# Kernel tuning notes

Measured on AMD Instinct MI355X. Metric: run time of the kernel, lower is better.

Reference implementation:

```python
import jax, jax.numpy as jnp
import numpy as np

B, S, DIM, H, D = 4, 2048, 1024, 16, 64
WINDOW = 512  # max_mem_segments * window_size


def _rotary_angles(seq_len, dim_head):
    inv_freq = 1.0 / (10000.0 ** (jnp.arange(0, dim_head, 2, dtype=jnp.float32) / dim_head))
    freqs = jnp.arange(seq_len, dtype=jnp.float32)[:, None] * inv_freq[None, :]  # [S, D/2]
    return jnp.repeat(freqs, 2, axis=-1)  # [S, D] interleaved


def _rotate_half(x):
    x1 = x[..., 0::2]
    x2 = x[..., 1::2]
    return jnp.stack((-x2, x1), axis=-1).reshape(x.shape)


def _apply_rotary(x, angles):
    # x: [b h n d], angles: [n d]
    return x * jnp.cos(angles) + _rotate_half(x) * jnp.sin(angles)


def setup_inputs() -> dict:
    key = jax.random.key(0)
    ks = jax.random.split(key, 7)
    tokens = jax.random.normal(ks[0], (B, S, DIM), dtype=jnp.float32)
    value_residual = jax.random.normal(ks[1], (B, H, S, D), dtype=jnp.float32)
    s = 0.02
    Wq = jax.random.normal(ks[2], (DIM, H * D), dtype=jnp.float32) * s
    Wkv = jax.random.normal(ks[3], (DIM, 2 * H * D), dtype=jnp.float32) * s
    Wout = jax.random.normal(ks[4], (H * D, DIM), dtype=jnp.float32) * s
    Wgate = jax.random.normal(ks[5], (DIM, H), dtype=jnp.float32) * s
    Wmix = jax.random.normal(ks[6], (DIM, H), dtype=jnp.float32) * s
    return {"tokens": tokens, "value_residual": value_residual, "Wq": Wq,
            "Wkv": Wkv, "Wout": Wout, "Wgate": Wgate, "Wmix": Wmix}


def reference(tokens, value_residual, Wq, Wkv, Wout, Wgate, Wmix):
    b, n, dim = tokens.shape
    scale = D ** -0.5

    def split_heads(t):  # [b n (h d)] -> [b h n d]
        return t.reshape(b, n, H, D).transpose(0, 2, 1, 3)

    q = split_heads(tokens @ Wq)
    kv = tokens @ Wkv
    k = split_heads(kv[..., : H * D])
    v = split_heads(kv[..., H * D:])

    q = q * scale

    # value-residual lerp: v.lerp(value_residual, mix)
    mix = jax.nn.sigmoid(jnp.einsum('bnd,dh->bhn', tokens, Wmix))[..., None]  # [b h n 1]
    v = v + (value_residual - v) * mix

    angles = _rotary_angles(n, D)
    q = _apply_rotary(q, angles)
    k = _apply_rotary(k, angles)

    sim = jnp.einsum('bhid,bhjd->bhij', q, k)

    # fixed-window causal mask: dist = i - j; masked if dist < 0 or dist > WINDOW
    pos = jnp.arange(n)
    dist = pos[:, None] - pos[None, :]
    mask = (dist < 0) | (dist > WINDOW)
    neg = -jnp.finfo(sim.dtype).max
    sim = jnp.where(mask[None, None], neg, sim)

    attn = jax.nn.softmax(sim, axis=-1)
    out = jnp.einsum('bhij,bhjd->bhid', attn, v)

    gates = jax.nn.sigmoid(jnp.einsum('bnd,dh->bhn', tokens, Wgate))[..., None]  # [b h n 1]
    out = out * gates

    out = out.transpose(0, 2, 1, 3).reshape(b, n, H * D)
    return out @ Wout
```

## Files before the change

kernel.cpp:

```cpp
#include <hip/hip_runtime.h>

#define NH 16
#define SLEN 2048
#define DMODEL 1024
#define DHEAD 64
#define WIN 512
#define NB 4

typedef unsigned short u16;
typedef unsigned int u32;
typedef unsigned long long u64;
typedef __attribute__((ext_vector_type(8))) __bf16 bf16x8;
typedef __attribute__((ext_vector_type(4))) float floatx4;

__device__ __forceinline__ float b2f(u32 bits16) {
  union { u32 i; float f; } x; x.i = bits16 << 16; return x.f;
}
__device__ __forceinline__ u16 f2b(float f) {
  union { float f; u32 i; } x; x.f = f;
  u32 r = x.i + 0x7fffu + ((x.i >> 16) & 1u);
  return (u16)(r >> 16);
}

__device__ __forceinline__ void gl2lds16(const u16* g, u16* l) {
  __builtin_amdgcn_global_load_lds(
      (const __attribute__((address_space(1))) unsigned int*)g,
      (__attribute__((address_space(3))) unsigned int*)l, 16, 0, 0);
}

template<int OFF>
__device__ __forceinline__ bf16x8 ldsr128(u32 addr) {
  bf16x8 r;
  if constexpr (OFF == 0)
    asm volatile("ds_read_b128 %0, %1" : "=v"(r) : "v"(addr));
  else
    asm volatile("ds_read_b128 %0, %1 offset:%2" : "=v"(r) : "v"(addr), "i"(OFF));
  return r;
}

#define WAIT_VM6   asm volatile("s_waitcnt vmcnt(6)" ::: "memory")
#define WAIT_VM0   asm volatile("s_waitcnt vmcnt(0)" ::: "memory")
#define WAIT_LGKM8 asm volatile("s_waitcnt lgkmcnt(8)" ::: "memory")
#define WAIT_LGKM0 asm volatile("s_waitcnt lgkmcnt(0)" ::: "memory")

__global__ __launch_bounds__(256) void prep_all(
    const float* __restrict__ tokens, const float* __restrict__ Wq,
    const float* __restrict__ Wkv, const float* __restrict__ Wout,
    const float* __restrict__ Wmix, const float* __restrict__ Wgate,
    u64* __restrict__ tokA64, u16* __restrict__ WqkvT, u16* __restrict__ WoutT,
    u16* __restrict__ Wmg, float2* __restrict__ rtab) {
  __shared__ u16 T[64][72];
  const int blk = blockIdx.x, tid = threadIdx.x;
  if (blk < 8192) {
    int i = blk * 256 + tid;
    float4 f = reinterpret_cast<const float4*>(tokens)[i];
    union { u16 u[4]; u64 ll; } pk;
    pk.u[0] = f2b(f.x); pk.u[1] = f2b(f.y); pk.u[2] = f2b(f.z); pk.u[3] = f2b(f.w);
    tokA64[i] = pk.ll;
  } else if (blk < 9216) {
    const float* src; u16* dst; int ld, nb, n0, k0;
    if (blk < 8960) {
      int tile = blk - 8192;
      n0 = (tile % 48) * 64; k0 = (tile / 48) * 64;
      if (n0 < 1024) { src = Wq; ld = 1024; nb = n0; }
      else { src = Wkv; ld = 2048; nb = n0 - 1024; }
      dst = WqkvT;
    } else {
      int tile = blk - 8960;
      n0 = (tile % 16) * 64; k0 = (tile / 16) * 64;
      src = Wout; ld = 1024; nb = n0; dst = WoutT;
    }
#pragma unroll
    for (int i = 0; i < 16; ++i) {
      int e = i * 256 + tid;
      int kr = e >> 6, nc = e & 63;
      T[kr][nc] = f2b(src[(size_t)(k0 + kr) * ld + nb + nc]);
    }
    __syncthreads();
#pragma unroll
    for (int i = 0; i < 16; ++i) {
      int e = i * 256 + tid;
      int nr = e >> 6, kc = e & 63;
      dst[(size_t)(n0 + nr) * 1024 + k0 + kc] = T[kc][nr];
    }
  } else if (blk < 9344) {
    int idx = (blk - 9216) * 256 + tid;
    int n = idx >> 10, k = idx & 1023;
    float v = (n < 16) ? Wmix[k * 16 + n] : Wgate[k * 16 + (n - 16)];
    Wmg[idx] = f2b(v);
  } else {
    int idx = (blk - 9344) * 256 + tid;
    int s = idx >> 5, t = idx & 31;
    float inv = __expf((float)t * -0.2878231366f);
    float ang = (float)s * inv;
    float sn, cs;
    __sincosf(ang, &sn, &cs);
    rtab[idx] = make_float2(cs, sn);
  }
}

__global__ __launch_bounds__(256) void mixgate_mfma(const u16* __restrict__ A,
    const u16* __restrict__ Wmg, float* __restrict__ mixws, float* __restrict__ gatews) {
  const int lane = threadIdx.x & 63, w = threadIdx.x >> 6;
  const int lm = lane & 15, quad = lane >> 4;
  const int row0 = (blockIdx.x * 4 + w) * 32;

  floatx4 acc[2][2];
#pragma unroll
  for (int i = 0; i < 2; ++i)
#pragma unroll
    for (int j = 0; j < 2; ++j)
      acc[i][j] = (floatx4){0.f, 0.f, 0.f, 0.f};

#pragma unroll 4
  for (int k0 = 0; k0 < 1024; k0 += 32) {
    bf16x8 af[2], bf[2];
#pragma unroll
    for (int mt = 0; mt < 2; ++mt)
      af[mt] = *reinterpret_cast<const bf16x8*>(
          &A[(size_t)(row0 + mt * 16 + lm) * 1024 + k0 + quad * 8]);
#pragma unroll
    for (int nt = 0; nt < 2; ++nt)
      bf[nt] = *reinterpret_cast<const bf16x8*>(
          &Wmg[(size_t)(nt * 16 + lm) * 1024 + k0 + quad * 8]);
#pragma unroll
    for (int mt = 0; mt < 2; ++mt)
#pragma unroll
      for (int nt = 0; nt < 2; ++nt)
        acc[mt][nt] = __builtin_amdgcn_mfma_f32_16x16x32_bf16(af[mt], bf[nt], acc[mt][nt], 0, 0, 0);
  }

#pragma unroll
  for (int mt = 0; mt < 2; ++mt)
#pragma unroll
    for (int r = 0; r < 4; ++r) {
      int grow = row0 + mt * 16 + quad * 4 + r;
      int b = grow >> 11, s = grow & 2047;
#pragma unroll
      for (int nt = 0; nt < 2; ++nt) {
        int n = nt * 16 + lm;
        float sig = 1.0f / (1.0f + __expf(-acc[mt][nt][r]));
        int h = n & 15;
        (n < 16 ? mixws : gatews)[(b * NH + h) * SLEN + s] = sig;
      }
    }
}

template<int MODE>
__global__ __launch_bounds__(512, 2) void gemm_pipe(
    const u16* __restrict__ A, const u16* __restrict__ Bt,
    float* __restrict__ C,
    u16* __restrict__ qws, u16* __restrict__ kws, u16* __restrict__ vws,
    const float* __restrict__ vres, const float* __restrict__ mixws,
    const float2* __restrict__ rtab, int N) {
  __shared__ u16 smem[73728];
  const int tid = threadIdx.x;
  const int nbx = N >> 7;
  const int wg = (blockIdx.x & 7) * (gridDim.x >> 3) + (blockIdx.x >> 3);
  const int bx = wg % nbx, by = wg / nbx;
  const int row0 = by * 256, col0 = bx * 128;
  const int w = tid >> 6, lane = tid & 63;
  const int wr = (w >> 1) * 64, wc = (w & 1) * 64;
  const int lm = lane & 15, quad = lane >> 4;
  const int NT = 16;
  const int sr = tid >> 3, sc = tid & 7;
  const int sl0 = (sr * 8 + sc) * 8;
  const u16* gA = A + (size_t)(row0 + sr) * 1024 + ((sc ^ (sr & 7)) << 3);
  const u16* gB = Bt + (size_t)(col0 + sr) * 1024 + ((sc ^ (sr & 7)) << 3);

  const u32 ldsbase = (u32)(size_t)(__attribute__((address_space(3))) u16*)smem;
  u32 arow[2], brow[2];
#pragma unroll
  for (int j = 0; j < 2; ++j) {
    u32 cslot = (u32)((j * 4 + quad) ^ (lm & 7));
    arow[j] = (u32)(wr + lm) * 128 + cslot * 16;
    brow[j] = (u32)(wc + lm) * 128 + cslot * 16;
  }

  floatx4 acc[4][4];
#pragma unroll
  for (int i = 0; i < 4; ++i)
#pragma unroll
    for (int j = 0; j < 4; ++j)
      acc[i][j] = (floatx4){0.f, 0.f, 0.f, 0.f};

  auto stage3 = [&](u16* Sa, u16* Sb, int ks, int half) {
    if (half == 0) {
      gl2lds16(gA + ks, Sa + sl0);
      gl2lds16(gA + 65536 + ks, Sa + 4096 + sl0);
      gl2lds16(gB + ks, Sb + sl0);
    } else {
      gl2lds16(gA + 131072 + ks, Sa + 8192 + sl0);
      gl2lds16(gA + 196608 + ks, Sa + 12288 + sl0);
      gl2lds16(gB + 65536 + ks, Sb + 4096 + sl0);
    }
  };

#pragma unroll
  for (int tt = 0; tt < 2; ++tt) {
    u16* Sa = smem + tt * 24576;
    u16* Sb = Sa + 16384;
    stage3(Sa, Sb, tt * 64, 0);
    stage3(Sa, Sb, tt * 64, 1);
  }

  int cur = 0;
  for (int t = 0; t < NT; ++t) {
    int sidx = cur + 2; if (sidx >= 3) sidx -= 3;
    u16* Sa = smem + sidx * 24576;
    u16* Sb = Sa + 16384;
    const int ks = (t + 2) << 6;
    const bool do_stage = t < NT - 2;
    const u32 abase = ldsbase + (u32)cur * 49152u;

    if (t < NT - 1) { WAIT_VM6; } else { WAIT_VM0; }
    __builtin_amdgcn_s_barrier();

    const u32 a0 = abase + arow[0], b0 = abase + 32768u + brow[0];
    const u32 a1 = abase + arow[1], b1 = abase + 32768u + brow[1];
    bf16x8 af0[4], bf0[4], af1[4], bf1[4];
    af0[0] = ldsr128<0>(a0);    af0[1] = ldsr128<2048>(a0);
    af0[2] = ldsr128<4096>(a0); af0[3] = ldsr128<6144>(a0);
    bf0[0] = ldsr128<0>(b0);    bf0[1] = ldsr128<2048>(b0);
    bf0[2] = ldsr128<4096>(b0); bf0[3] = ldsr128<6144>(b0);
    af1[0] = ldsr128<0>(a1);    af1[1] = ldsr128<2048>(a1);
    af1[2] = ldsr128<4096>(a1); af1[3] = ldsr128<6144>(a1);
    bf1[0] = ldsr128<0>(b1);    bf1[1] = ldsr128<2048>(b1);
    bf1[2] = ldsr128<4096>(b1); bf1[3] = ldsr128<6144>(b1);
    if (do_stage) { stage3(Sa, Sb, ks, 0); stage3(Sa, Sb, ks, 1); }
    __builtin_amdgcn_sched_barrier(0);
    WAIT_LGKM8;
    __builtin_amdgcn_sched_barrier(0);
    __builtin_amdgcn_s_setprio(1);
#pragma unroll
    for (int mt = 0; mt < 4; ++mt)
#pragma unroll
      for (int nt = 0; nt < 4; ++nt)
        acc[mt][nt] = __builtin_amdgcn_mfma_f32_16x16x32_bf16(
            af0[mt], bf0[nt], acc[mt][nt], 0, 0, 0);
    __builtin_amdgcn_s_setprio(0);
    WAIT_LGKM0;
    __builtin_amdgcn_sched_barrier(0);
    __builtin_amdgcn_s_setprio(1);
#pragma unroll
    for (int mt = 0; mt < 4; ++mt)
#pragma unroll
      for (int nt = 0; nt < 4; ++nt)
        acc[mt][nt] = __builtin_amdgcn_mfma_f32_16x16x32_bf16(
            af1[mt], bf1[nt], acc[mt][nt], 0, 0, 0);
    __builtin_amdgcn_s_setprio(0);

    cur += 1; if (cur >= 3) cur -= 3;
  }

  if (MODE == 0) {
#pragma unroll
    for (int mt = 0; mt < 4; ++mt)
#pragma unroll
      for (int r = 0; r < 4; ++r) {
        int grow = row0 + wr + mt * 16 + quad * 4 + r;
#pragma unroll
        for (int nt = 0; nt < 4; ++nt)
          C[(size_t)grow * N + col0 + wc + nt * 16 + lm] = acc[mt][nt][r];
      }
  } else {
    const int seg = col0 >> 10;
    if (seg < 2) {
      u16* dst = seg ? kws : qws;
      const float qs = seg ? 1.0f : 0.125f;
      const int colb = (col0 & 1023) + wc;
#pragma unroll
      for (int mt = 0; mt < 4; ++mt)
#pragma unroll
        for (int r = 0; r < 4; ++r) {
          int sg = row0 + wr + mt * 16 + quad * 4 + r;
          int b = sg >> 11, s = sg & 2047;
#pragma unroll
          for (int nt = 0; nt < 4; ++nt) {
            int nn = colb + nt * 16 + lm;
            int h = nn >> 6, d = nn & 63;
            float val = acc[mt][nt][r] * qs;
            float2 cs = rtab[(s << 5) + (d >> 1)];
            float partner = __shfl_xor(val, 1);
            float o = (d & 1) ? fmaf(val, cs.x, partner * cs.y)
                              : fmaf(val, cs.x, -partner * cs.y);
            dst[((size_t)((b * NH + h) * SLEN + s)) * 64 + d] = f2b(o);
          }
        }
    } else {
      const int h0 = (col0 - 2048) >> 6;
      const int p = (w & 1);
      const int b = row0 >> 11, s0 = row0 & 2047;
      const int bh = b * NH + h0 + p;
      u16 (*Vt)[264] = reinterpret_cast<u16(*)[264]>(smem + p * 16896);
      __syncthreads();
#pragma unroll
      for (int mt = 0; mt < 4; ++mt)
#pragma unroll
        for (int nt = 0; nt < 4; ++nt) {
          const int d = nt * 16 + lm;
          const int sl = wr + mt * 16 + quad * 4;
          union { u16 u[4]; u64 ll; } pk;
#pragma unroll
          for (int r = 0; r < 4; ++r) {
            int s = s0 + sl + r;
            float val = acc[mt][nt][r];
            float mv = mixws[bh * SLEN + s];
            float o = val + (vres[((size_t)(bh * SLEN + s)) * 64 + d] - val) * mv;
            pk.u[r] = f2b(o);
          }
          *reinterpret_cast<u64*>(&Vt[d][sl]) = pk.ll;
        }
      __syncthreads();
#pragma unroll
      for (int it = 0; it < 8; ++it) {
        int idx = it * 512 + tid;
        int ph = idx >> 11, rem = idx & 2047;
        int d = rem >> 5, ch = rem & 31;
        const u16* src = smem + ph * 16896 + d * 264 + ch * 8;
        u16* dst = vws + ((size_t)((b * NH + h0 + ph) * 64 + d)) * SLEN + s0 + ch * 8;
        *reinterpret_cast<uint4*>(dst) = *reinterpret_cast<const uint4*>(src);
      }
    }
  }
}

__global__ __launch_bounds__(256) void attn_mfma_kernel(
    const u16* __restrict__ q, const u16* __restrict__ k, const u16* __restrict__ vt,
    const float* __restrict__ gate, u16* __restrict__ X) {
  __shared__ u16 Ks[4096];
  __shared__ u16 Vs[4096];
  __shared__ u16 Ps[4][16][72];
  const int tid = threadIdx.x;
  const int w = tid >> 6, lane = tid & 63;
  const int lm = lane & 15, quad = lane >> 4;
  const int blk = blockIdx.x;
  const int qt = blk & 31;
  const int h = (blk >> 5) & 15;
  const int b = blk >> 9;
  const int bh = b * NH + h;
  const int q0 = qt * 64;
  const size_t kqbase = (size_t)bh * SLEN * 64;
  const size_t vbase  = (size_t)bh * 64 * SLEN;

  bf16x8 qf[2];
  {
    const u16* qrow = q + kqbase + (size_t)(q0 + w * 16 + lm) * 64;
    qf[0] = *reinterpret_cast<const bf16x8*>(qrow + quad * 8);
    qf[1] = *reinterpret_cast<const bf16x8*>(qrow + 32 + quad * 8);
  }

  floatx4 o[4];
#pragma unroll
  for (int nt = 0; nt < 4; ++nt) o[nt] = (floatx4){0.f, 0.f, 0.f, 0.f};
  float lsum = 0.f;
  const int iq = q0 + w * 16 + lm;

  const int c_first = (q0 >= WIN) ? ((q0 - WIN) >> 6) : 0;
  const int c_last = q0 >> 6;
  const int vrow = tid >> 3, vcol = (tid & 7) * 8;
  for (int c = c_first; c <= c_last; ++c) {
    const int c0 = c << 6;
    __syncthreads();
    {
      const u16* kg = k + kqbase + (size_t)c0 * 64;
      gl2lds16(kg + tid * 8, Ks + tid * 8);
      gl2lds16(kg + 2048 + tid * 8, Ks + 2048 + tid * 8);
      const u16* vg = vt + vbase + c0;
      gl2lds16(vg + (size_t)vrow * SLEN + vcol, Vs + tid * 8);
      gl2lds16(vg + (size_t)(vrow + 32) * SLEN + vcol, Vs + 2048 + tid * 8);
    }
    __syncthreads();

    floatx4 st[4];
#pragma unroll
    for (int mt = 0; mt < 4; ++mt) {
      bf16x8 kf0 = *reinterpret_cast<const bf16x8*>(&Ks[(mt * 16 + lm) * 64 + quad * 8]);
      bf16x8 kf1 = *reinterpret_cast<const bf16x8*>(&Ks[(mt * 16 + lm) * 64 + 32 + quad * 8]);
      st[mt] = __builtin_amdgcn_mfma_f32_16x16x32_bf16(kf0, qf[0],
                   (floatx4){0.f, 0.f, 0.f, 0.f}, 0, 0, 0);
      st[mt] = __builtin_amdgcn_mfma_f32_16x16x32_bf16(kf1, qf[1], st[mt], 0, 0, 0);
    }
    const bool need_mask = (c == c_first && q0 >= WIN) || (c == c_last);
    if (need_mask) {
#pragma unroll
      for (int mt = 0; mt < 4; ++mt)
#pragma unroll
        for (int r = 0; r < 4; ++r) {
          int j = c0 + mt * 16 + quad * 4 + r;
          bool valid = (j <= iq) && (j >= iq - WIN);
          if (!valid) st[mt][r] = -3.0e38f;
        }
    }
    float p[4][4], psum = 0.f;
#pragma unroll
    for (int mt = 0; mt < 4; ++mt)
#pragma unroll
      for (int r = 0; r < 4; ++r) {
        p[mt][r] = __expf(st[mt][r]);
        psum += p[mt][r];
      }
    psum += __shfl_xor(psum, 16);
    psum += __shfl_xor(psum, 32);
    lsum += psum;
#pragma unroll
    for (int mt = 0; mt < 4; ++mt) {
      union { u16 u[4]; u64 ll; } pk;
#pragma unroll
      for (int r = 0; r < 4; ++r) pk.u[r] = f2b(p[mt][r]);
      *reinterpret_cast<u64*>(&Ps[w][lm][mt * 16 + quad * 4]) = pk.ll;
    }
    __builtin_amdgcn_wave_barrier();
    __builtin_amdgcn_s_waitcnt(0xC07F);
    __builtin_amdgcn_wave_barrier();
    bf16x8 af0 = *reinterpret_cast<const bf16x8*>(&Ps[w][lm][quad * 8]);
    bf16x8 af1 = *reinterpret_cast<const bf16x8*>(&Ps[w][lm][32 + quad * 8]);
#pragma unroll
    for (int nt = 0; nt < 4; ++nt) {
      bf16x8 vf0 = *reinterpret_cast<const bf16x8*>(&Vs[(nt * 16 + lm) * 64 + quad * 8]);
      bf16x8 vf1 = *reinterpret_cast<const bf16x8*>(&Vs[(nt * 16 + lm) * 64 + 32 + quad * 8]);
      o[nt] = __builtin_amdgcn_mfma_f32_16x16x32_bf16(af0, vf0, o[nt], 0, 0, 0);
      o[nt] = __builtin_amdgcn_mfma_f32_16x16x32_bf16(af1, vf1, o[nt], 0, 0, 0);
    }
  }
  float linv[4], g[4];
#pragma unroll
  for (int r = 0; r < 4; ++r) {
    linv[r] = 1.0f / __shfl(lsum, quad * 4 + r);
    g[r] = gate[bh * SLEN + q0 + w * 16 + quad * 4 + r];
  }
#pragma unroll
  for (int r = 0; r < 4; ++r) {
    int i = q0 + w * 16 + quad * 4 + r;
    u16* xrow = X + ((size_t)(b * SLEN + i)) * 1024 + h * 64;
#pragma unroll
    for (int nt = 0; nt < 4; ++nt)
      xrow[nt * 16 + lm] = f2b(o[nt][r] * linv[r] * g[r]);
  }
}

extern "C" void kernel_launch(void* const* d_in, const int* in_sizes, int n_in,
                              void* d_out, int out_size, void* d_ws, size_t ws_size,
                              hipStream_t stream) {
  (void)in_sizes; (void)n_in; (void)out_size; (void)ws_size;
  const float* tokens = (const float*)d_in[0];
  const float* vres   = (const float*)d_in[1];
  const float* Wq     = (const float*)d_in[2];
  const float* Wkv    = (const float*)d_in[3];
  const float* Wout   = (const float*)d_in[4];
  const float* Wgate  = (const float*)d_in[5];
  const float* Wmix   = (const float*)d_in[6];
  float* out = (float*)d_out;

  char* p = (char*)d_ws;
  auto alloc = [&](size_t bytes) { char* r = p; p += (bytes + 255) & ~(size_t)255; return r; };
  u16*  tokA   = (u16*)alloc(8192ull * 1024 * 2);
  u16*  WqkvT  = (u16*)alloc(3072ull * 1024 * 2);
  u16*  WoutT  = (u16*)alloc(1024ull * 1024 * 2);
  u16*  Wmg    = (u16*)alloc(32ull * 1024 * 2);
  float2* rtab = (float2*)alloc(65536ull * 8);
  u16*  qws    = (u16*)alloc(8388608ull * 2);
  u16*  kws    = (u16*)alloc(8388608ull * 2);
  u16*  vws    = (u16*)alloc(8388608ull * 2);
  u16*  Xws    = (u16*)alloc(8388608ull * 2);
  float* mixws = (float*)alloc(131072ull * 4);
  float* gatews= (float*)alloc(131072ull * 4);

  prep_all<<<9600, 256, 0, stream>>>(tokens, Wq, Wkv, Wout, Wmix, Wgate,
      (u64*)tokA, WqkvT, WoutT, Wmg, rtab);
  mixgate_mfma<<<64, 256, 0, stream>>>(tokA, Wmg, mixws, gatews);
  gemm_pipe<1><<<768, 512, 0, stream>>>(tokA, WqkvT, nullptr,
      qws, kws, vws, vres, mixws, rtab, 3072);
  attn_mfma_kernel<<<2048, 256, 0, stream>>>(qws, kws, vws, gatews, Xws);
  gemm_pipe<0><<<256, 512, 0, stream>>>(Xws, WoutT, out,
      nullptr, nullptr, nullptr, nullptr, nullptr, nullptr, 1024);
}
```

Measured before the change: 285.7 us.

## Double-buffer K/V tiles with swizzled LDS layout in attention kernel

```diff
diff --git a/kernel.cpp b/kernel.cpp
--- a/kernel.cpp
+++ b/kernel.cpp
@@ -328,9 +328,9 @@
 __global__ __launch_bounds__(256) void attn_mfma_kernel(
     const u16* __restrict__ q, const u16* __restrict__ k, const u16* __restrict__ vt,
     const float* __restrict__ gate, u16* __restrict__ X) {
-  __shared__ u16 Ks[4096];
-  __shared__ u16 Vs[4096];
-  __shared__ u16 Ps[4][16][72];
+  __shared__ __align__(16) u16 Ks[2][4096];
+  __shared__ __align__(16) u16 Vs[2][4096];
+  __shared__ __align__(16) u16 Ps[4][16][72];
   const int tid = threadIdx.x;
   const int w = tid >> 6, lane = tid & 63;
   const int lm = lane & 15, quad = lane >> 4;
@@ -358,29 +358,55 @@
 
   const int c_first = (q0 >= WIN) ? ((q0 - WIN) >> 6) : 0;
   const int c_last = q0 >> 6;
-  const int vrow = tid >> 3, vcol = (tid & 7) * 8;
+
+  const int sr = tid >> 3;
+  const int scz = ((tid & 7) ^ (sr & 7)) * 8;
+  const u32 ksbase = (u32)(size_t)(__attribute__((address_space(3))) u16*)&Ks[0][0];
+  const u32 vsbase = (u32)(size_t)(__attribute__((address_space(3))) u16*)&Vs[0][0];
+  const u32 psbase = (u32)(size_t)(__attribute__((address_space(3))) u16*)&Ps[0][0][0];
+  const int rxa8 = lm & 7;
+  const u32 rowoff = (u32)lm * 128 + (u32)((quad ^ rxa8) * 16);
+  const u32 paddr = psbase + (u32)(w * 16 + lm) * 144 + (u32)quad * 16;
+
+  auto stage = [&](int c, int buf) {
+    const u16* kg = k + kqbase + (size_t)(c << 6) * 64;
+    const u16* vg = vt + vbase + (c << 6);
+    u16* Kd = &Ks[buf][0]; u16* Vd = &Vs[buf][0];
+    gl2lds16(kg + sr * 64 + scz, Kd + tid * 8);
+    gl2lds16(kg + (sr + 32) * 64 + scz, Kd + 2048 + tid * 8);
+    gl2lds16(vg + (size_t)sr * SLEN + scz, Vd + tid * 8);
+    gl2lds16(vg + (size_t)(sr + 32) * SLEN + scz, Vd + 2048 + tid * 8);
+  };
+
+  stage(c_first, 0);
+  int cur = 0;
   for (int c = c_first; c <= c_last; ++c) {
     const int c0 = c << 6;
     __syncthreads();
-    {
-      const u16* kg = k + kqbase + (size_t)c0 * 64;
-      gl2lds16(kg + tid * 8, Ks + tid * 8);
-      gl2lds16(kg + 2048 + tid * 8, Ks + 2048 + tid * 8);
-      const u16* vg = vt + vbase + c0;
-      gl2lds16(vg + (size_t)vrow * SLEN + vcol, Vs + tid * 8);
-      gl2lds16(vg + (size_t)(vrow + 32) * SLEN + vcol, Vs + 2048 + tid * 8);
-    }
-    __syncthreads();
-
+    if (c < c_last) stage(c + 1, cur ^ 1);
+
+    const u32 kof = ksbase + (u32)(cur << 13) + rowoff;
+    const u32 kof4 = kof ^ 64u;
+    bf16x8 k00 = ldsr128<0>(kof),     k01 = ldsr128<2048>(kof),
+           k02 = ldsr128<4096>(kof),  k03 = ldsr128<6144>(kof);
+    bf16x8 k10 = ldsr128<0>(kof4),    k11 = ldsr128<2048>(kof4),
+           k12 = ldsr128<4096>(kof4), k13 = ldsr128<6144>(kof4);
+    __builtin_amdgcn_sched_barrier(0);
+    WAIT_LGKM0;
+    __builtin_amdgcn_sched_barrier(0);
     floatx4 st[4];
-#pragma unroll
-    for (int mt = 0; mt < 4; ++mt) {
-      bf16x8 kf0 = *reinterpret_cast<const bf16x8*>(&Ks[(mt * 16 + lm) * 64 + quad * 8]);
-      bf16x8 kf1 = *reinterpret_cast<const bf16x8*>(&Ks[(mt * 16 + lm) * 64 + 32 + quad * 8]);
-      st[mt] = __builtin_amdgcn_mfma_f32_16x16x32_bf16(kf0, qf[0],
-                   (floatx4){0.f, 0.f, 0.f, 0.f}, 0, 0, 0);
-      st[mt] = __builtin_amdgcn_mfma_f32_16x16x32_bf16(kf1, qf[1], st[mt], 0, 0, 0);
-    }
+    const floatx4 z4 = (floatx4){0.f, 0.f, 0.f, 0.f};
+    __builtin_amdgcn_s_setprio(1);
+    st[0] = __builtin_amdgcn_mfma_f32_16x16x32_bf16(k00, qf[0], z4, 0, 0, 0);
+    st[0] = __builtin_amdgcn_mfma_f32_16x16x32_bf16(k10, qf[1], st[0], 0, 0, 0);
+    st[1] = __builtin_amdgcn_mfma_f32_16x16x32_bf16(k01, qf[0], z4, 0, 0, 0);
+    st[1] = __builtin_amdgcn_mfma_f32_16x16x32_bf16(k11, qf[1], st[1], 0, 0, 0);
+    st[2] = __builtin_amdgcn_mfma_f32_16x16x32_bf16(k02, qf[0], z4, 0, 0, 0);
+    st[2] = __builtin_amdgcn_mfma_f32_16x16x32_bf16(k12, qf[1], st[2], 0, 0, 0);
+    st[3] = __builtin_amdgcn_mfma_f32_16x16x32_bf16(k03, qf[0], z4, 0, 0, 0);
+    st[3] = __builtin_amdgcn_mfma_f32_16x16x32_bf16(k13, qf[1], st[3], 0, 0, 0);
+    __builtin_amdgcn_s_setprio(0);
+
     const bool need_mask = (c == c_first && q0 >= WIN) || (c == c_last);
     if (need_mask) {
 #pragma unroll
@@ -413,15 +439,29 @@
     __builtin_amdgcn_wave_barrier();
     __builtin_amdgcn_s_waitcnt(0xC07F);
     __builtin_amdgcn_wave_barrier();
-    bf16x8 af0 = *reinterpret_cast<const bf16x8*>(&Ps[w][lm][quad * 8]);
-    bf16x8 af1 = *reinterpret_cast<const bf16x8*>(&Ps[w][lm][32 + quad * 8]);
-#pragma unroll
-    for (int nt = 0; nt < 4; ++nt) {
-      bf16x8 vf0 = *reinterpret_cast<const bf16x8*>(&Vs[(nt * 16 + lm) * 64 + quad * 8]);
-      bf16x8 vf1 = *reinterpret_cast<const bf16x8*>(&Vs[(nt * 16 + lm) * 64 + 32 + quad * 8]);
-      o[nt] = __builtin_amdgcn_mfma_f32_16x16x32_bf16(af0, vf0, o[nt], 0, 0, 0);
-      o[nt] = __builtin_amdgcn_mfma_f32_16x16x32_bf16(af1, vf1, o[nt], 0, 0, 0);
-    }
+
+    bf16x8 pa0 = ldsr128<0>(paddr), pa1 = ldsr128<64>(paddr);
+    const u32 vof = vsbase + (u32)(cur << 13) + rowoff;
+    const u32 vof4 = vof ^ 64u;
+    bf16x8 v00 = ldsr128<0>(vof),     v01 = ldsr128<2048>(vof),
+           v02 = ldsr128<4096>(vof),  v03 = ldsr128<6144>(vof);
+    bf16x8 v10 = ldsr128<0>(vof4),    v11 = ldsr128<2048>(vof4),
+           v12 = ldsr128<4096>(vof4), v13 = ldsr128<6144>(vof4);
+    __builtin_amdgcn_sched_barrier(0);
+    WAIT_LGKM0;
+    __builtin_amdgcn_sched_barrier(0);
+    __builtin_amdgcn_s_setprio(1);
+    o[0] = __builtin_amdgcn_mfma_f32_16x16x32_bf16(pa0, v00, o[0], 0, 0, 0);
+    o[0] = __builtin_amdgcn_mfma_f32_16x16x32_bf16(pa1, v10, o[0], 0, 0, 0);
+    o[1] = __builtin_amdgcn_mfma_f32_16x16x32_bf16(pa0, v01, o[1], 0, 0, 0);
+    o[1] = __builtin_amdgcn_mfma_f32_16x16x32_bf16(pa1, v11, o[1], 0, 0, 0);
+    o[2] = __builtin_amdgcn_mfma_f32_16x16x32_bf16(pa0, v02, o[2], 0, 0, 0);
+    o[2] = __builtin_amdgcn_mfma_f32_16x16x32_bf16(pa1, v12, o[2], 0, 0, 0);
+    o[3] = __builtin_amdgcn_mfma_f32_16x16x32_bf16(pa0, v03, o[3], 0, 0, 0);
+    o[3] = __builtin_amdgcn_mfma_f32_16x16x32_bf16(pa1, v13, o[3], 0, 0, 0);
+    __builtin_amdgcn_s_setprio(0);
+
+    cur ^= 1;
   }
   float linv[4], g[4];
 #pragma unroll
```

After: 273.7 us. 1.04x faster.
